# Optimization experiments

Measured on AMD Instinct MI355X. Metric: run time of the kernel, lower is better.

## Reference

```python
import jax, jax.numpy as jnp
import numpy as np

N_NODES = 50000
N_EDGES = 800000
DIM_IN = 128
DIM_OUT = 64
HEADS = 4
NEG_SLOPE = 0.2


def setup_inputs() -> dict:
    key = jax.random.key(0)
    k_x, k_e, k_w, k_a = jax.random.split(key, 4)
    x = jax.random.normal(k_x, (N_NODES, DIM_IN), dtype=jnp.float32)
    edge_index = jax.random.randint(k_e, (2, N_EDGES), 0, N_NODES, dtype=jnp.int32)
    # Stacked per-head params: W (Linear(dim_in, dim_out, bias=False)) and
    # a (Linear(2*dim_out, 1, bias=False)) for each of HEADS heads.
    W = jax.random.normal(k_w, (HEADS, DIM_IN, DIM_OUT), dtype=jnp.float32) * (1.0 / np.sqrt(DIM_IN))
    a = jax.random.normal(k_a, (HEADS, 2 * DIM_OUT), dtype=jnp.float32) * (1.0 / np.sqrt(2 * DIM_OUT))
    return {"x": x, "edge_index": edge_index, "W": W, "a": a}


def _gat_forward(x, W, a, edge_index):
    src = edge_index[0]  # segment for softmax / scatter target
    dst = edge_index[1]  # node whose features are gathered (x_j)
    # h: [N, H, D]
    h = jnp.einsum('nd,hdo->nho', x, W)
    a_i = a[:, :DIM_OUT]   # [H, D] applied to x_i
    a_j = a[:, DIM_OUT:]   # [H, D] applied to x_j
    # per-node attention logit halves: [N, H]
    s_i = jnp.einsum('nhd,hd->nh', h, a_i)
    s_j = jnp.einsum('nhd,hd->nh', h, a_j)
    e = jax.nn.leaky_relu(s_i[src] + s_j[dst], NEG_SLOPE)  # [E, H]
    # segment softmax over edges grouped by src node
    m = jax.ops.segment_max(e, src, num_segments=N_NODES)  # [N, H]
    ex = jnp.exp(e - m[src])
    denom = jax.ops.segment_sum(ex, src, num_segments=N_NODES)  # [N, H]
    att = ex / denom[src]  # [E, H]
    # weighted scatter-sum of gathered features: [N, H, D]
    msgs = att[:, :, None] * h[dst]
    h_prime = jax.ops.segment_sum(msgs, src, num_segments=N_NODES)
    # concat=False -> mean over heads
    return jnp.mean(h_prime, axis=1)  # [N, D]


def reference(x, edge_index, W, a):
    return _gat_forward(x, W, a, edge_index)
```

## Files before the change

kernel.cpp:

```cpp
#include <hip/hip_runtime.h>
#include <hip/hip_bf16.h>

#define N_NODES 50000
#define N_EDGES 800000
#define DIM_IN  128
#define DIM_OUT 64
#define HEADS   4
#define NEG_SLOPE 0.2f
#define NPB 32
#define GEMM_BLOCKS ((N_NODES + NPB - 1) / NPB)
#define N_PAD (GEMM_BLOCKS * NPB)
#define PAD 64
#define CHUNKS 128
#define EPC (N_EDGES / CHUNKS)
#define RANGES 128
#define RSPAN 391
#define HTOT (RANGES * CHUNKS)
#define XROW 136
#define LTROW 260

typedef __attribute__((ext_vector_type(8))) short short8;
typedef __attribute__((ext_vector_type(4))) short short4v;
typedef __attribute__((ext_vector_type(4))) float f32x4;

__device__ __forceinline__ unsigned int f2bf(float f) {
    unsigned int u = __float_as_uint(f);
    return (u + 0x7FFFu + ((u >> 16) & 1u)) >> 16;
}
__device__ __forceinline__ float bf2f(unsigned int b) {
    return __uint_as_float(b << 16);
}

__global__ __launch_bounds__(256) void pack_hist_kernel(
    const float* __restrict__ W, unsigned short* __restrict__ Wph,
    unsigned short* __restrict__ Wpl, const int* __restrict__ ei,
    unsigned int* __restrict__ histT)
{
    const int b = blockIdx.x;
    const int t = threadIdx.x;
    if (b < 16) {
        const int i = b * 256 + t;
        const int lane = i & 63, nt = (i >> 6) & 3, kc = (i >> 8) & 3, h = (i >> 10) & 3;
        const int col = lane & 15, quad = lane >> 4;
        unsigned short hv[8], lv[8];
#pragma unroll
        for (int j = 0; j < 8; ++j) {
            const int k = kc * 32 + quad * 8 + j;
            const int n = nt * 16 + col;
            const float f = W[h * (DIM_IN * DIM_OUT) + k * DIM_OUT + n];
            const unsigned int hb = f2bf(f);
            hv[j] = (unsigned short)hb;
            lv[j] = (unsigned short)f2bf(f - bf2f(hb));
        }
        *(short8*)(Wph + (size_t)i * 8) = *(short8*)hv;
        *(short8*)(Wpl + (size_t)i * 8) = *(short8*)lv;
        return;
    }
    __shared__ unsigned int h4[4][RANGES];
    const int c = b - 16;
    const int w = t >> 6;
    for (int i = t; i < 4 * RANGES; i += 256) ((unsigned int*)h4)[i] = 0u;
    __syncthreads();
    const int* srcp = ei + c * EPC;
    for (int e = t; e < EPC; e += 256) {
        const int s = srcp[e];
        atomicAdd(&h4[w][s / RSPAN], 1u);
    }
    __syncthreads();
    if (t < RANGES)
        histT[t * CHUNKS + c] = h4[0][t] + h4[1][t] + h4[2][t] + h4[3][t];
}

__global__ __launch_bounds__(256) void scan_gemm_kernel(
    const float* __restrict__ x, const unsigned short* __restrict__ Wph,
    const unsigned short* __restrict__ Wpl, const float* __restrict__ a,
    unsigned short* __restrict__ h2, float* __restrict__ s_i, float* __restrict__ s_j,
    const unsigned int* __restrict__ histT, unsigned int* __restrict__ S)
{
    __shared__ __align__(16) unsigned char smem[2 * NPB * XROW * 2];
    const int b = blockIdx.x;
    const int t = threadIdx.x;

    if (b == 0) {
        unsigned int* part = (unsigned int*)smem;
        const uint4* H4 = (const uint4*)histT;
        unsigned int sum = 0;
#pragma unroll
        for (int q = 0; q < 16; ++q) {
            const uint4 v = H4[t * 16 + q];
            sum += v.x + v.y + v.z + v.w;
        }
        part[t] = sum;
        __syncthreads();
        for (int off = 1; off < 256; off <<= 1) {
            const unsigned int v = (t >= off) ? part[t - off] : 0u;
            __syncthreads();
            part[t] += v;
            __syncthreads();
        }
        unsigned int run = part[t] - sum;
        uint4* S4 = (uint4*)S;
#pragma unroll
        for (int q = 0; q < 16; ++q) {
            const uint4 v = H4[t * 16 + q];
            uint4 o;
            o.x = run; run += v.x;
            o.y = run; run += v.y;
            o.z = run; run += v.z;
            o.w = run; run += v.w;
            S4[t * 16 + q] = o;
        }
        return;
    }

    short* xh = (short*)smem;
    short* xl = xh + NPB * XROW;
    const int nb = (b - 1) * NPB;

    {
        const float4* xg = (const float4*)x;
        const int base = nb * (DIM_IN / 4);
        const int limit = N_NODES * (DIM_IN / 4);
#pragma unroll
        for (int r = 0; r < 4; ++r) {
            const int idx = t + 256 * r;
            const int gi = base + idx;
            float4 v = {0.f, 0.f, 0.f, 0.f};
            if (gi < limit) v = xg[gi];
            const int node = idx >> 5;
            const int dg = (idx & 31) * 4;
            unsigned short hs[4], ls[4];
            const float fv[4] = {v.x, v.y, v.z, v.w};
#pragma unroll
            for (int c = 0; c < 4; ++c) {
                const unsigned int hb = f2bf(fv[c]);
                hs[c] = (unsigned short)hb;
                ls[c] = (unsigned short)f2bf(fv[c] - bf2f(hb));
            }
            *(short4v*)(xh + node * XROW + dg) = *(short4v*)hs;
            *(short4v*)(xl + node * XROW + dg) = *(short4v*)ls;
        }
    }
    __syncthreads();

    const int w = t >> 6;
    const int lane = t & 63;
    const int col = lane & 15, quad = lane >> 4;

    f32x4 acc[2][4];
#pragma unroll
    for (int mt = 0; mt < 2; ++mt)
#pragma unroll
        for (int nt = 0; nt < 4; ++nt) acc[mt][nt] = (f32x4){0.f, 0.f, 0.f, 0.f};

    const short8* Bh = (const short8*)Wph;
    const short8* Bl = (const short8*)Wpl;
#pragma unroll
    for (int kc = 0; kc < 4; ++kc) {
        const short8 ah0 = *(const short8*)(xh + (0 * 16 + col) * XROW + kc * 32 + quad * 8);
        const short8 al0 = *(const short8*)(xl + (0 * 16 + col) * XROW + kc * 32 + quad * 8);
        const short8 ah1 = *(const short8*)(xh + (1 * 16 + col) * XROW + kc * 32 + quad * 8);
        const short8 al1 = *(const short8*)(xl + (1 * 16 + col) * XROW + kc * 32 + quad * 8);
#pragma unroll
        for (int nt = 0; nt < 4; ++nt) {
            const int fi = ((w * 4 + kc) * 4 + nt) * 64 + lane;
            const short8 bh = Bh[fi];
            const short8 bl = Bl[fi];
            acc[0][nt] = __builtin_amdgcn_mfma_f32_16x16x32_bf16(ah0, bh, acc[0][nt], 0, 0, 0);
            acc[0][nt] = __builtin_amdgcn_mfma_f32_16x16x32_bf16(al0, bh, acc[0][nt], 0, 0, 0);
            acc[0][nt] = __builtin_amdgcn_mfma_f32_16x16x32_bf16(ah0, bl, acc[0][nt], 0, 0, 0);
            acc[1][nt] = __builtin_amdgcn_mfma_f32_16x16x32_bf16(ah1, bh, acc[1][nt], 0, 0, 0);
            acc[1][nt] = __builtin_amdgcn_mfma_f32_16x16x32_bf16(al1, bh, acc[1][nt], 0, 0, 0);
            acc[1][nt] = __builtin_amdgcn_mfma_f32_16x16x32_bf16(ah1, bl, acc[1][nt], 0, 0, 0);
        }
    }

    float aiv[4], ajv[4];
#pragma unroll
    for (int nt = 0; nt < 4; ++nt) {
        aiv[nt] = a[w * (2 * DIM_OUT) + nt * 16 + col];
        ajv[nt] = a[w * (2 * DIM_OUT) + DIM_OUT + nt * 16 + col];
    }
#pragma unroll
    for (int mt = 0; mt < 2; ++mt) {
#pragma unroll
        for (int r = 0; r < 4; ++r) {
            float pi = 0.f, pj = 0.f;
#pragma unroll
            for (int nt = 0; nt < 4; ++nt) {
                pi = fmaf(acc[mt][nt][r], aiv[nt], pi);
                pj = fmaf(acc[mt][nt][r], ajv[nt], pj);
            }
#pragma unroll
            for (int off = 8; off > 0; off >>= 1) {
                pi += __shfl_down(pi, off, 16);
                pj += __shfl_down(pj, off, 16);
            }
            if (col == 0) {
                const int n = nb + mt * 16 + quad * 4 + r;
                s_i[n * HEADS + w] = pi;
                s_j[n * HEADS + w] = pj;
            }
        }
    }
    __syncthreads();

    short* lt = (short*)smem;
#pragma unroll
    for (int mt = 0; mt < 2; ++mt)
#pragma unroll
        for (int nt = 0; nt < 4; ++nt)
#pragma unroll
            for (int r = 0; r < 4; ++r)
                lt[(mt * 16 + quad * 4 + r) * LTROW + (nt * 16 + col) * 4 + w] =
                    (short)f2bf(acc[mt][nt][r]);
    __syncthreads();

    uint2* hg = (uint2*)(h2 + (size_t)nb * (DIM_OUT * HEADS));
#pragma unroll
    for (int r = 0; r < 8; ++r) {
        const int idx = t + 256 * r;
        const int node = idx >> 6;
        const int wo = idx & 63;
        hg[idx] = *(const uint2*)(lt + node * LTROW + wo * 4);
    }
}

__global__ __launch_bounds__(512) void bucket_kernel(
    const int* __restrict__ ei, const unsigned int* __restrict__ S,
    unsigned int* __restrict__ ebuf)
{
    __shared__ unsigned int cur[RANGES];
    const int c = blockIdx.x;
    const int t = threadIdx.x;
    if (t < RANGES) cur[t] = S[t * CHUNKS + c];
    __syncthreads();
    const int* srcp = ei + c * EPC;
    const int* dstp = ei + N_EDGES + c * EPC;
    for (int e = t; e < EPC; e += 512) {
        const int s = srcp[e];
        const int d = dstp[e];
        const int r = s / RSPAN;
        const unsigned int pos = atomicAdd(&cur[r], 1u);
        ebuf[pos] = ((unsigned int)(s - r * RSPAN) << 16) | (unsigned int)d;
    }
}

__global__ __launch_bounds__(512) void csr_kernel(
    const unsigned int* __restrict__ ebuf, const unsigned int* __restrict__ S,
    unsigned short* __restrict__ sdst, int* __restrict__ cursor)
{
    __shared__ unsigned int cur[RSPAN];
    const int r = blockIdx.x;
    const int t = threadIdx.x;
    const unsigned int j0 = S[r * CHUNKS];
    const unsigned int j1 = (r + 1 < RANGES) ? S[(r + 1) * CHUNKS] : N_EDGES;
    for (int i = t; i < RSPAN; i += 512) cur[i] = 0u;
    __syncthreads();
    for (unsigned int e = j0 + t; e < j1; e += 512) {
        const unsigned int v = ebuf[e];
        const unsigned int sl = v >> 16;
        const unsigned int d = v & 0xFFFFu;
        const unsigned int slot = atomicAdd(&cur[sl], 1u);
        if (slot < PAD) sdst[(size_t)(r * RSPAN + sl) * PAD + slot] = (unsigned short)d;
    }
    __syncthreads();
    for (int i = t; i < RSPAN; i += 512) {
        const int n = r * RSPAN + i;
        if (n < N_NODES) cursor[n] = (int)cur[i];
    }
}

__global__ __launch_bounds__(256) void fused_kernel(
    const int* __restrict__ cursor, const unsigned short* __restrict__ sdst,
    const float* __restrict__ s_i, const float* __restrict__ s_j,
    const unsigned short* __restrict__ h2, float* __restrict__ out)
{
    __shared__ float4 att_s[4][64];
    __shared__ int    dst_s[4][64];
    const int wid = (blockIdx.x * 256 + threadIdx.x) >> 6;
    const int w = (threadIdx.x >> 6) & 3;
    const int lane = threadIdx.x & 63;
    if (wid >= N_NODES) return;
    const int n = wid;
    const int d = min(cursor[n], PAD);
    const int start = n * PAD;

    float acc = 0.f;
    if (d > 0) {
        const float4 si = *(const float4*)(s_i + n * HEADS);
        float4 m4 = {-INFINITY, -INFINITY, -INFINITY, -INFINITY};
        float4 cz = {-INFINITY, -INFINITY, -INFINITY, -INFINITY};
        int cdst = 0;
        if (lane < d) {
            cdst = (int)sdst[start + lane];
            const float4 sj = *(const float4*)(s_j + cdst * HEADS);
            float z0 = si.x + sj.x, z1 = si.y + sj.y, z2 = si.z + sj.z, z3 = si.w + sj.w;
            cz.x = z0 >= 0.f ? z0 : NEG_SLOPE * z0;
            cz.y = z1 >= 0.f ? z1 : NEG_SLOPE * z1;
            cz.z = z2 >= 0.f ? z2 : NEG_SLOPE * z2;
            cz.w = z3 >= 0.f ? z3 : NEG_SLOPE * z3;
            m4 = cz;
        }
#pragma unroll
        for (int off = 32; off > 0; off >>= 1) {
            m4.x = fmaxf(m4.x, __shfl_xor(m4.x, off, 64));
            m4.y = fmaxf(m4.y, __shfl_xor(m4.y, off, 64));
            m4.z = fmaxf(m4.z, __shfl_xor(m4.z, off, 64));
            m4.w = fmaxf(m4.w, __shfl_xor(m4.w, off, 64));
        }
        float4 ex = {0.f, 0.f, 0.f, 0.f};
        if (lane < d) {
            ex.x = __expf(cz.x - m4.x);
            ex.y = __expf(cz.y - m4.y);
            ex.z = __expf(cz.z - m4.z);
            ex.w = __expf(cz.w - m4.w);
        }
        float4 sm = ex;
#pragma unroll
        for (int off = 32; off > 0; off >>= 1) {
            sm.x += __shfl_xor(sm.x, off, 64);
            sm.y += __shfl_xor(sm.y, off, 64);
            sm.z += __shfl_xor(sm.z, off, 64);
            sm.w += __shfl_xor(sm.w, off, 64);
        }
        if (lane < d) {
            att_s[w][lane] = make_float4(ex.x / sm.x, ex.y / sm.y, ex.z / sm.z, ex.w / sm.w);
            dst_s[w][lane] = cdst;
        }

        const unsigned short* hbase = h2 + lane * HEADS;
        int e = 0;
        for (; e + 8 <= d; e += 8) {
            uint2 hv[8];
            float4 at[8];
#pragma unroll
            for (int q = 0; q < 8; ++q) {
                const int dd = dst_s[w][e + q];
                at[q] = att_s[w][e + q];
                hv[q] = *(const uint2*)(hbase + (size_t)dd * (DIM_OUT * HEADS));
            }
#pragma unroll
            for (int q = 0; q < 8; ++q) {
                acc += at[q].x * bf2f(hv[q].x & 0xFFFFu) + at[q].y * bf2f(hv[q].x >> 16)
                     + at[q].z * bf2f(hv[q].y & 0xFFFFu) + at[q].w * bf2f(hv[q].y >> 16);
            }
        }
        for (; e + 4 <= d; e += 4) {
            uint2 hv[4];
            float4 at[4];
#pragma unroll
            for (int q = 0; q < 4; ++q) {
                const int dd = dst_s[w][e + q];
                at[q] = att_s[w][e + q];
                hv[q] = *(const uint2*)(hbase + (size_t)dd * (DIM_OUT * HEADS));
            }
#pragma unroll
            for (int q = 0; q < 4; ++q) {
                acc += at[q].x * bf2f(hv[q].x & 0xFFFFu) + at[q].y * bf2f(hv[q].x >> 16)
                     + at[q].z * bf2f(hv[q].y & 0xFFFFu) + at[q].w * bf2f(hv[q].y >> 16);
            }
        }
        for (; e < d; ++e) {
            const int dd = dst_s[w][e];
            const float4 a4 = att_s[w][e];
            const uint2 hv = *(const uint2*)(hbase + (size_t)dd * (DIM_OUT * HEADS));
            acc += a4.x * bf2f(hv.x & 0xFFFFu) + a4.y * bf2f(hv.x >> 16)
                 + a4.z * bf2f(hv.y & 0xFFFFu) + a4.w * bf2f(hv.y >> 16);
        }
    }
    out[n * DIM_OUT + lane] = 0.25f * acc;
}

extern "C" void kernel_launch(void* const* d_in, const int* in_sizes, int n_in,
                              void* d_out, int out_size, void* d_ws, size_t ws_size,
                              hipStream_t stream) {
    const float* x  = (const float*)d_in[0];
    const int*   ei = (const int*)d_in[1];
    const float* W  = (const float*)d_in[2];
    const float* a  = (const float*)d_in[3];
    float* out = (float*)d_out;

    char* ws = (char*)d_ws;
    size_t off = 0;
    auto alloc = [&](size_t bytes) { void* p = ws + off; off = (off + bytes + 511) & ~size_t(511); return p; };
    unsigned short* h2  = (unsigned short*)alloc(sizeof(unsigned short) * N_PAD * DIM_OUT * HEADS);
    float* s_i    = (float*)alloc(sizeof(float) * N_PAD * HEADS);
    float* s_j    = (float*)alloc(sizeof(float) * N_PAD * HEADS);
    int*   cursor = (int*)alloc(sizeof(int) * N_NODES);
    unsigned short* sdst = (unsigned short*)alloc(sizeof(unsigned short) * N_NODES * PAD);
    unsigned int* histT  = (unsigned int*)alloc(sizeof(unsigned int) * HTOT);
    unsigned int* S      = (unsigned int*)alloc(sizeof(unsigned int) * HTOT);
    unsigned int* ebuf   = (unsigned int*)alloc(sizeof(unsigned int) * N_EDGES);
    unsigned short* Wph  = (unsigned short*)alloc(sizeof(unsigned short) * HEADS * DIM_IN * DIM_OUT);
    unsigned short* Wpl  = (unsigned short*)alloc(sizeof(unsigned short) * HEADS * DIM_IN * DIM_OUT);

    pack_hist_kernel<<<16 + CHUNKS, 256, 0, stream>>>(W, Wph, Wpl, ei, histT);

    scan_gemm_kernel<<<1 + GEMM_BLOCKS, 256, 0, stream>>>(x, Wph, Wpl, a, h2, s_i, s_j, histT, S);

    bucket_kernel<<<CHUNKS, 512, 0, stream>>>(ei, S, ebuf);

    csr_kernel<<<RANGES, 512, 0, stream>>>(ebuf, S, sdst, cursor);

    const int fb = (N_NODES * 64 + 255) / 256;
    fused_kernel<<<fb, 256, 0, stream>>>(cursor, sdst, s_i, s_j, h2, out);
}
```

Before: 181.5 us.

## Restructure edge bucketing into per-chunk local sort and overlap CSR with GEMM

Replaces the global histogram, scan and scatter (three dependent launches) with a per-chunk block-local counting sort that writes chunk-local offsets. The CSR build then walks 128 chunk sub-ranges per range and runs in the same launch as the GEMM blocks, so the sparse preprocessing overlaps with the dense projection. This removes two kernel launches and the global scan dependency. In exchange the CSR blocks read scattered, fragmented segments, and the edge order within a node's list changes.

```diff
diff --git a/kernel.cpp b/kernel.cpp
--- a/kernel.cpp
+++ b/kernel.cpp
@@ -15,9 +15,10 @@
 #define EPC (N_EDGES / CHUNKS)
 #define RANGES 128
 #define RSPAN 391
-#define HTOT (RANGES * CHUNKS)
+#define OPITCH 132
 #define XROW 136
 #define LTROW 260
+#define SMEM_BYTES (2 * NPB * XROW * 2)
 
 typedef __attribute__((ext_vector_type(8))) short short8;
 typedef __attribute__((ext_vector_type(4))) short short4v;
@@ -31,91 +32,79 @@
     return __uint_as_float(b << 16);
 }
 
-__global__ __launch_bounds__(256) void pack_hist_kernel(
+__device__ __forceinline__ void packW_role(
+    int i, const float* __restrict__ W,
+    unsigned short* __restrict__ Wph, unsigned short* __restrict__ Wpl)
+{
+    const int lane = i & 63, nt = (i >> 6) & 3, kc = (i >> 8) & 3, h = (i >> 10) & 3;
+    const int col = lane & 15, quad = lane >> 4;
+    unsigned short hv[8], lv[8];
+#pragma unroll
+    for (int j = 0; j < 8; ++j) {
+        const int k = kc * 32 + quad * 8 + j;
+        const int n = nt * 16 + col;
+        const float f = W[h * (DIM_IN * DIM_OUT) + k * DIM_OUT + n];
+        const unsigned int hb = f2bf(f);
+        hv[j] = (unsigned short)hb;
+        lv[j] = (unsigned short)f2bf(f - bf2f(hb));
+    }
+    *(short8*)(Wph + (size_t)i * 8) = *(short8*)hv;
+    *(short8*)(Wpl + (size_t)i * 8) = *(short8*)lv;
+}
+
+__global__ __launch_bounds__(512) void sort_kernel(
     const float* __restrict__ W, unsigned short* __restrict__ Wph,
     unsigned short* __restrict__ Wpl, const int* __restrict__ ei,
-    unsigned int* __restrict__ histT)
+    unsigned int* __restrict__ offT, unsigned int* __restrict__ ebuf)
 {
     const int b = blockIdx.x;
     const int t = threadIdx.x;
-    if (b < 16) {
-        const int i = b * 256 + t;
-        const int lane = i & 63, nt = (i >> 6) & 3, kc = (i >> 8) & 3, h = (i >> 10) & 3;
-        const int col = lane & 15, quad = lane >> 4;
-        unsigned short hv[8], lv[8];
-#pragma unroll
-        for (int j = 0; j < 8; ++j) {
-            const int k = kc * 32 + quad * 8 + j;
-            const int n = nt * 16 + col;
-            const float f = W[h * (DIM_IN * DIM_OUT) + k * DIM_OUT + n];
-            const unsigned int hb = f2bf(f);
-            hv[j] = (unsigned short)hb;
-            lv[j] = (unsigned short)f2bf(f - bf2f(hb));
-        }
-        *(short8*)(Wph + (size_t)i * 8) = *(short8*)hv;
-        *(short8*)(Wpl + (size_t)i * 8) = *(short8*)lv;
-        return;
-    }
-    __shared__ unsigned int h4[4][RANGES];
-    const int c = b - 16;
-    const int w = t >> 6;
-    for (int i = t; i < 4 * RANGES; i += 256) ((unsigned int*)h4)[i] = 0u;
+    if (b < 8) { packW_role(b * 512 + t, W, Wph, Wpl); return; }
+
+    __shared__ unsigned int hist[RANGES];
+    __shared__ unsigned int scn[RANGES + 1];
+    __shared__ unsigned int cur[RANGES];
+    const int c = b - 8;
+    if (t < RANGES) hist[t] = 0u;
     __syncthreads();
     const int* srcp = ei + c * EPC;
-    for (int e = t; e < EPC; e += 256) {
+    const int* dstp = ei + N_EDGES + c * EPC;
+    for (int e = t; e < EPC; e += 512) atomicAdd(&hist[srcp[e] / RSPAN], 1u);
+    __syncthreads();
+    if (t < RANGES) scn[t + 1] = hist[t];
+    if (t == 0) scn[0] = 0u;
+    __syncthreads();
+    for (int off = 1; off < RANGES; off <<= 1) {
+        unsigned int v = 0u;
+        if (t < RANGES && (t + 1) > off) v = scn[t + 1 - off];
+        __syncthreads();
+        if (t < RANGES) scn[t + 1] += v;
+        __syncthreads();
+    }
+    if (t < RANGES) {
+        cur[t] = scn[t];
+        offT[c * OPITCH + t] = (unsigned int)(c * EPC) + scn[t];
+    }
+    if (t == 0) offT[c * OPITCH + RANGES] = (unsigned int)((c + 1) * EPC);
+    __syncthreads();
+    unsigned int* eb = ebuf + (size_t)c * EPC;
+    for (int e = t; e < EPC; e += 512) {
         const int s = srcp[e];
-        atomicAdd(&h4[w][s / RSPAN], 1u);
-    }
-    __syncthreads();
-    if (t < RANGES)
-        histT[t * CHUNKS + c] = h4[0][t] + h4[1][t] + h4[2][t] + h4[3][t];
-}
-
-__global__ __launch_bounds__(256) void scan_gemm_kernel(
-    const float* __restrict__ x, const unsigned short* __restrict__ Wph,
-    const unsigned short* __restrict__ Wpl, const float* __restrict__ a,
-    unsigned short* __restrict__ h2, float* __restrict__ s_i, float* __restrict__ s_j,
-    const unsigned int* __restrict__ histT, unsigned int* __restrict__ S)
-{
-    __shared__ __align__(16) unsigned char smem[2 * NPB * XROW * 2];
-    const int b = blockIdx.x;
-    const int t = threadIdx.x;
-
-    if (b == 0) {
-        unsigned int* part = (unsigned int*)smem;
-        const uint4* H4 = (const uint4*)histT;
-        unsigned int sum = 0;
-#pragma unroll
-        for (int q = 0; q < 16; ++q) {
-            const uint4 v = H4[t * 16 + q];
-            sum += v.x + v.y + v.z + v.w;
-        }
-        part[t] = sum;
-        __syncthreads();
-        for (int off = 1; off < 256; off <<= 1) {
-            const unsigned int v = (t >= off) ? part[t - off] : 0u;
-            __syncthreads();
-            part[t] += v;
-            __syncthreads();
-        }
-        unsigned int run = part[t] - sum;
-        uint4* S4 = (uint4*)S;
-#pragma unroll
-        for (int q = 0; q < 16; ++q) {
-            const uint4 v = H4[t * 16 + q];
-            uint4 o;
-            o.x = run; run += v.x;
-            o.y = run; run += v.y;
-            o.z = run; run += v.z;
-            o.w = run; run += v.w;
-            S4[t * 16 + q] = o;
-        }
-        return;
-    }
-
-    short* xh = (short*)smem;
+        const int d = dstp[e];
+        const int r = s / RSPAN;
+        const unsigned int pos = atomicAdd(&cur[r], 1u);
+        eb[pos] = ((unsigned int)(s - r * RSPAN) << 16) | (unsigned int)d;
+    }
+}
+
+__device__ __forceinline__ void gemm_role(
+    int nb, int t, const float* __restrict__ x,
+    const unsigned short* __restrict__ Wph, const unsigned short* __restrict__ Wpl,
+    const float* __restrict__ a, unsigned short* __restrict__ h2,
+    float* __restrict__ s_i, float* __restrict__ s_j, void* smemv)
+{
+    short* xh = (short*)smemv;
     short* xl = xh + NPB * XROW;
-    const int nb = (b - 1) * NPB;
 
     {
         const float4* xg = (const float4*)x;
@@ -205,7 +194,7 @@
     }
     __syncthreads();
 
-    short* lt = (short*)smem;
+    short* lt = (short*)smemv;
 #pragma unroll
     for (int mt = 0; mt < 2; ++mt)
 #pragma unroll
@@ -226,49 +215,48 @@
     }
 }
 
-__global__ __launch_bounds__(512) void bucket_kernel(
-    const int* __restrict__ ei, const unsigned int* __restrict__ S,
-    unsigned int* __restrict__ ebuf)
-{
-    __shared__ unsigned int cur[RANGES];
-    const int c = blockIdx.x;
+__global__ __launch_bounds__(256) void csr_gemm_kernel(
+    const float* __restrict__ x, const unsigned short* __restrict__ Wph,
+    const unsigned short* __restrict__ Wpl, const float* __restrict__ a,
+    unsigned short* __restrict__ h2, float* __restrict__ s_i, float* __restrict__ s_j,
+    const unsigned int* __restrict__ offT, const unsigned int* __restrict__ ebuf,
+    unsigned short* __restrict__ sdst, int* __restrict__ cursor)
+{
+    __shared__ __align__(16) unsigned char smem[SMEM_BYTES];
+    const int b = blockIdx.x;
     const int t = threadIdx.x;
-    if (t < RANGES) cur[t] = S[t * CHUNKS + c];
-    __syncthreads();
-    const int* srcp = ei + c * EPC;
-    const int* dstp = ei + N_EDGES + c * EPC;
-    for (int e = t; e < EPC; e += 512) {
-        const int s = srcp[e];
-        const int d = dstp[e];
-        const int r = s / RSPAN;
-        const unsigned int pos = atomicAdd(&cur[r], 1u);
-        ebuf[pos] = ((unsigned int)(s - r * RSPAN) << 16) | (unsigned int)d;
-    }
-}
-
-__global__ __launch_bounds__(512) void csr_kernel(
-    const unsigned int* __restrict__ ebuf, const unsigned int* __restrict__ S,
-    unsigned short* __restrict__ sdst, int* __restrict__ cursor)
-{
-    __shared__ unsigned int cur[RSPAN];
-    const int r = blockIdx.x;
-    const int t = threadIdx.x;
-    const unsigned int j0 = S[r * CHUNKS];
-    const unsigned int j1 = (r + 1 < RANGES) ? S[(r + 1) * CHUNKS] : N_EDGES;
-    for (int i = t; i < RSPAN; i += 512) cur[i] = 0u;
-    __syncthreads();
-    for (unsigned int e = j0 + t; e < j1; e += 512) {
-        const unsigned int v = ebuf[e];
-        const unsigned int sl = v >> 16;
-        const unsigned int d = v & 0xFFFFu;
-        const unsigned int slot = atomicAdd(&cur[sl], 1u);
-        if (slot < PAD) sdst[(size_t)(r * RSPAN + sl) * PAD + slot] = (unsigned short)d;
-    }
-    __syncthreads();
-    for (int i = t; i < RSPAN; i += 512) {
-        const int n = r * RSPAN + i;
-        if (n < N_NODES) cursor[n] = (int)cur[i];
-    }
+
+    if (b < RANGES) {
+        unsigned int* cur  = (unsigned int*)smem;
+        unsigned int* offA = cur + RSPAN;
+        unsigned int* offB = offA + CHUNKS;
+        const int r = b;
+        for (int i = t; i < RSPAN; i += 256) cur[i] = 0u;
+        if (t < CHUNKS) {
+            offA[t] = offT[t * OPITCH + r];
+            offB[t] = offT[t * OPITCH + r + 1];
+        }
+        __syncthreads();
+        const int w = t >> 6, lane = t & 63;
+        for (int c = w; c < CHUNKS; c += 4) {
+            const unsigned int j0 = offA[c], j1 = offB[c];
+            for (unsigned int e = j0 + lane; e < j1; e += 64) {
+                const unsigned int v = ebuf[e];
+                const unsigned int sl = v >> 16;
+                const unsigned int d = v & 0xFFFFu;
+                const unsigned int slot = atomicAdd(&cur[sl], 1u);
+                if (slot < PAD) sdst[(size_t)(r * RSPAN + sl) * PAD + slot] = (unsigned short)d;
+            }
+        }
+        __syncthreads();
+        for (int i = t; i < RSPAN; i += 256) {
+            const int n = r * RSPAN + i;
+            if (n < N_NODES) cursor[n] = (int)cur[i];
+        }
+        return;
+    }
+
+    gemm_role((b - RANGES) * NPB, t, x, Wph, Wpl, a, h2, s_i, s_j, smem);
 }
 
 __global__ __launch_bounds__(256) void fused_kernel(
@@ -278,11 +266,10 @@
 {
     __shared__ float4 att_s[4][64];
     __shared__ int    dst_s[4][64];
-    const int wid = (blockIdx.x * 256 + threadIdx.x) >> 6;
     const int w = (threadIdx.x >> 6) & 3;
     const int lane = threadIdx.x & 63;
-    if (wid >= N_NODES) return;
-    const int n = wid;
+    const int n = blockIdx.x * 4 + w;
+    if (n >= N_NODES) return;
     const int d = min(cursor[n], PAD);
     const int start = n * PAD;
 
@@ -389,20 +376,16 @@
     float* s_j    = (float*)alloc(sizeof(float) * N_PAD * HEADS);
     int*   cursor = (int*)alloc(sizeof(int) * N_NODES);
     unsigned short* sdst = (unsigned short*)alloc(sizeof(unsigned short) * N_NODES * PAD);
-    unsigned int* histT  = (unsigned int*)alloc(sizeof(unsigned int) * HTOT);
-    unsigned int* S      = (unsigned int*)alloc(sizeof(unsigned int) * HTOT);
+    unsigned int* offT   = (unsigned int*)alloc(sizeof(unsigned int) * CHUNKS * OPITCH);
     unsigned int* ebuf   = (unsigned int*)alloc(sizeof(unsigned int) * N_EDGES);
     unsigned short* Wph  = (unsigned short*)alloc(sizeof(unsigned short) * HEADS * DIM_IN * DIM_OUT);
     unsigned short* Wpl  = (unsigned short*)alloc(sizeof(unsigned short) * HEADS * DIM_IN * DIM_OUT);
 
-    pack_hist_kernel<<<16 + CHUNKS, 256, 0, stream>>>(W, Wph, Wpl, ei, histT);
-
-    scan_gemm_kernel<<<1 + GEMM_BLOCKS, 256, 0, stream>>>(x, Wph, Wpl, a, h2, s_i, s_j, histT, S);
-
-    bucket_kernel<<<CHUNKS, 512, 0, stream>>>(ei, S, ebuf);
-
-    csr_kernel<<<RANGES, 512, 0, stream>>>(ebuf, S, sdst, cursor);
-
-    const int fb = (N_NODES * 64 + 255) / 256;
+    sort_kernel<<<8 + CHUNKS, 512, 0, stream>>>(W, Wph, Wpl, ei, offT, ebuf);
+
+    csr_gemm_kernel<<<RANGES + GEMM_BLOCKS, 256, 0, stream>>>(
+        x, Wph, Wpl, a, h2, s_i, s_j, offT, ebuf, sdst, cursor);
+
+    const int fb = (N_NODES + 3) / 4;
     fused_kernel<<<fb, 256, 0, stream>>>(cursor, sdst, s_i, s_j, h2, out);
 }
```

Result: faster. 169.8 us (-6.4%).
